# Performance work log

Hardware: AMD Instinct MI355X
Metric: run time of the kernel (lower is better)

## Reference

```python
import jax, jax.numpy as jnp
import numpy as np

B, C, T, N, KS = 32, 64, 12, 1024, 3
OUT = 64


def _gconv_layer(x, Lk, theta, b):
    # x: [B, i, T, N], Lk: [ks, N, N], theta: [i, c, ks], b: [1, c, 1, 1]
    x_c = jnp.einsum('knm,bitm->bitkn', Lk, x)        # graph diffusion
    x_gc = jnp.einsum('iok,bitkn->botn', theta, x_c) + b  # channel mix + bias
    return jax.nn.relu(x_gc + x)                      # residual + relu


def setup_inputs() -> dict:
    key = jax.random.key(0)
    ks = jax.random.split(key, 8)
    return {
        'x': jax.random.normal(ks[0], (B, C, T, N), dtype=jnp.float32),
        'Lk': jax.random.normal(ks[1], (KS, N, N), dtype=jnp.float32) * 0.05,
        'theta1': jax.random.normal(ks[2], (C, C, KS), dtype=jnp.float32) * 0.1,
        'b1': jax.random.normal(ks[3], (1, C, 1, 1), dtype=jnp.float32) * 0.1,
        'theta2': jax.random.normal(ks[4], (C, C, KS), dtype=jnp.float32) * 0.1,
        'b2': jax.random.normal(ks[5], (1, C, 1, 1), dtype=jnp.float32) * 0.1,
        'fc_w': jax.random.normal(ks[6], (OUT, C), dtype=jnp.float32) * 0.1,
        'fc_b': jax.random.normal(ks[7], (OUT,), dtype=jnp.float32) * 0.1,
    }


def reference(x, Lk, theta1, b1, theta2, b2, fc_w, fc_b):
    x1 = _gconv_layer(x, Lk, theta1, b1)
    x2 = _gconv_layer(x1, Lk, theta2, b2)
    # permute [B, c, T, N] -> [B, T, N, c], then Linear(c -> OUT)
    x2 = jnp.transpose(x2, (0, 2, 3, 1))
    return x2 @ fc_w.T + fc_b
```

## Files before the change

kernel.cpp:

```cpp
#include <hip/hip_runtime.h>

typedef unsigned short ushort_t;
typedef unsigned long long u64;
typedef short short8 __attribute__((ext_vector_type(8)));
typedef float f32x4 __attribute__((ext_vector_type(4)));

#define B_   32
#define C_   64
#define T_   12
#define N_   1024
#define KS_  3
#define KC_  3072
#define RPB  768
#define NT_  48
#define BM_  192
#define LBUF 57344
#define ABYT 24576
#define BPLN 16384

__device__ __forceinline__ float bf2f(ushort_t u) {
  union { unsigned u; float f; } v; v.u = ((unsigned)u) << 16; return v.f;
}
__device__ __forceinline__ ushort_t f2bf(float f) {
  union { float f; unsigned u; } v; v.f = f;
  unsigned r = v.u + 0x7FFFu + ((v.u >> 16) & 1u);
  return (ushort_t)(r >> 16);
}

__device__ __forceinline__ void gload16(const ushort_t* g, ushort_t* l) {
  __builtin_amdgcn_global_load_lds(
      (const __attribute__((address_space(1))) unsigned int*)g,
      (__attribute__((address_space(3))) unsigned int*)l, 16, 0, 0);
}

__global__ void prep_th(const float* __restrict__ th1, const float* __restrict__ th2,
                        ushort_t* __restrict__ out) {
  int id = blockIdx.x * 256 + threadIdx.x;
  if (id >= 24576) return;
  int l = id / 12288, rem = id % 12288;
  int k = rem / 4096;
  int o = (rem >> 6) & 63;
  int i = rem & 63;
  const float* th = l ? th2 : th1;
  out[id] = f2bf(th[(i * 64 + o) * 3 + k]);
}

__global__ void prep_bt(const float* __restrict__ Lk, ushort_t* __restrict__ Bt) {
  int id = blockIdx.x * 256 + threadIdx.x;
  int k = id >> 17, rem = id & 131071;
  int n = rem >> 7, mc = rem & 127;
  int m = mc << 3;
  const float* src = Lk + ((k * N_ + n) * N_ + m);
  float4 v0 = *(const float4*)src;
  float4 v1 = *(const float4*)(src + 4);
  short8 o8;
  o8[0] = (short)f2bf(v0.x); o8[1] = (short)f2bf(v0.y);
  o8[2] = (short)f2bf(v0.z); o8[3] = (short)f2bf(v0.w);
  o8[4] = (short)f2bf(v1.x); o8[5] = (short)f2bf(v1.y);
  o8[6] = (short)f2bf(v1.z); o8[7] = (short)f2bf(v1.w);
  *(short8*)&Bt[n * KC_ + k * N_ + m] = o8;
}

template<int IN_BF16>
__global__ __launch_bounds__(256, 2)
void mix_mfma(const void* __restrict__ in, const ushort_t* __restrict__ thA,
              ushort_t* __restrict__ Y, int b0) {
  const int bid = blockIdx.x;
  const int mq = bid & 3;
  const int bt = bid >> 2;
  const int bl = bt / 12, t = bt % 12;
  const int b = b0 + bl;
  const int tid = threadIdx.x;
  const int wv = tid >> 6, lane = tid & 63;
  const int l15 = lane & 15, l4 = lane >> 4;
  const int m0 = mq * 256 + wv * 64;

  const ushort_t* xg_b = (const ushort_t*)in;
  const float*    xg_f = (const float*)in;

  short8 bfr[4][2];
  #pragma unroll
  for (int mf = 0; mf < 4; ++mf) {
    const int m = m0 + mf * 16 + l15;
    #pragma unroll
    for (int ks = 0; ks < 2; ++ks) {
      #pragma unroll
      for (int j = 0; j < 8; ++j) {
        const int i = ks * 32 + l4 * 8 + j;
        const size_t adr = ((size_t)(b * C_ + i) * T_ + t) * N_ + m;
        ushort_t v = IN_BF16 ? xg_b[adr] : f2bf(xg_f[adr]);
        bfr[mf][ks][j] = (short)v;
      }
    }
  }

  const size_t rbase = (size_t)(bt * C_);
  #pragma unroll
  for (int k = 0; k < 3; ++k) {
    short8 afr[4][2];
    #pragma unroll
    for (int of = 0; of < 4; ++of)
      #pragma unroll
      for (int ks = 0; ks < 2; ++ks)
        afr[of][ks] = *(const short8*)&thA[(size_t)(k * 64 + of * 16 + l15) * 64 + ks * 32 + l4 * 8];

    f32x4 acc[4][4] = {};
    #pragma unroll
    for (int ks = 0; ks < 2; ++ks)
      #pragma unroll
      for (int of = 0; of < 4; ++of)
        #pragma unroll
        for (int mf = 0; mf < 4; ++mf)
          acc[of][mf] = __builtin_amdgcn_mfma_f32_16x16x32_bf16(afr[of][ks], bfr[mf][ks], acc[of][mf], 0, 0, 0);

    #pragma unroll
    for (int of = 0; of < 4; ++of)
      #pragma unroll
      for (int mf = 0; mf < 4; ++mf)
        #pragma unroll
        for (int r = 0; r < 4; ++r) {
          const int o = of * 16 + l4 * 4 + r;
          Y[(rbase + o) * KC_ + k * N_ + m0 + mf * 16 + l15] = f2bf(acc[of][mf][r]);
        }
  }
}


#define MFMA12(g)                                                                           \
  acc[3*(g)+0][0] = __builtin_amdgcn_mfma_f32_16x16x32_bf16(a0, b0, acc[3*(g)+0][0],0,0,0); \
  acc[3*(g)+0][1] = __builtin_amdgcn_mfma_f32_16x16x32_bf16(a0, b1, acc[3*(g)+0][1],0,0,0); \
  acc[3*(g)+0][2] = __builtin_amdgcn_mfma_f32_16x16x32_bf16(a0, b2, acc[3*(g)+0][2],0,0,0); \
  acc[3*(g)+0][3] = __builtin_amdgcn_mfma_f32_16x16x32_bf16(a0, b3, acc[3*(g)+0][3],0,0,0); \
  acc[3*(g)+1][0] = __builtin_amdgcn_mfma_f32_16x16x32_bf16(a1, b0, acc[3*(g)+1][0],0,0,0); \
  acc[3*(g)+1][1] = __builtin_amdgcn_mfma_f32_16x16x32_bf16(a1, b1, acc[3*(g)+1][1],0,0,0); \
  acc[3*(g)+1][2] = __builtin_amdgcn_mfma_f32_16x16x32_bf16(a1, b2, acc[3*(g)+1][2],0,0,0); \
  acc[3*(g)+1][3] = __builtin_amdgcn_mfma_f32_16x16x32_bf16(a1, b3, acc[3*(g)+1][3],0,0,0); \
  acc[3*(g)+2][0] = __builtin_amdgcn_mfma_f32_16x16x32_bf16(a2, b0, acc[3*(g)+2][0],0,0,0); \
  acc[3*(g)+2][1] = __builtin_amdgcn_mfma_f32_16x16x32_bf16(a2, b1, acc[3*(g)+2][1],0,0,0); \
  acc[3*(g)+2][2] = __builtin_amdgcn_mfma_f32_16x16x32_bf16(a2, b2, acc[3*(g)+2][2],0,0,0); \
  acc[3*(g)+2][3] = __builtin_amdgcn_mfma_f32_16x16x32_bf16(a2, b3, acc[3*(g)+2][3],0,0,0);

#define STAGE_A(kt, j) gload16(gA##j + (size_t)(kt) * 64,                                   \
    (ushort_t*)(lp + (((kt) & 1) ? LBUF : 0) + (j) * 8192 + wofs))
#define STAGE_B(kt, j) gload16(gB##j + (size_t)(kt) * 64,                                   \
    (ushort_t*)(lp + (((kt) & 1) ? LBUF : 0) + ABYT + (j) * 8192 + wofs))

#define LD8(p) (*(const short8*)(p))

template<int RES_BF16>
__global__ __launch_bounds__(512, 2)
void gemm8p(const ushort_t* __restrict__ Y, const ushort_t* __restrict__ Bt,
            const void* __restrict__ res, const float* __restrict__ bias,
            ushort_t* __restrict__ outb, int batch0) {
  const int nwg = gridDim.x;
  int orig = blockIdx.x;
  int q8 = nwg >> 3;
  int wg = (orig & 7) * q8 + (orig >> 3);
  const int mtile = wg >> 2, ntile = wg & 3;

  const int tid = threadIdx.x;
  const int wid = tid >> 6, lane = tid & 63;
  const int wm = wid >> 2, wn = wid & 3;
  const int l15 = lane & 15, l4 = lane >> 4;

  __shared__ ushort_t LDSU[LBUF];
  char* lp = (char*)LDSU;

  const int row0 = mtile * BM_;
  const int n0 = ntile * 256;
  const int wofs = wid * 1024;

  const int lam = lane >> 2, lc = lane & 3;
  const ushort_t *gA0, *gA1, *gA2, *gB0, *gB1, *gB2, *gB3;
  {
    int p, s, row, colel;
    p = 0 * 128 + wid * 16 + lam; s = p >= 192 ? 1 : 0; row = p - s * 192;
    colel = (lc * 8) ^ (((row >> 3) & 1) << 4);
    gA0 = Y + (size_t)(row0 + row) * KC_ + s * 32 + colel;
    p = 1 * 128 + wid * 16 + lam; s = p >= 192 ? 1 : 0; row = p - s * 192;
    colel = (lc * 8) ^ (((row >> 3) & 1) << 4);
    gA1 = Y + (size_t)(row0 + row) * KC_ + s * 32 + colel;
    p = 2 * 128 + wid * 16 + lam; s = p >= 192 ? 1 : 0; row = p - s * 192;
    colel = (lc * 8) ^ (((row >> 3) & 1) << 4);
    gA2 = Y + (size_t)(row0 + row) * KC_ + s * 32 + colel;
    p = 0 * 128 + wid * 16 + lam; s = p >> 8; row = p & 255;
    colel = (lc * 8) ^ (((row >> 3) & 1) << 4);
    gB0 = Bt + (size_t)(n0 + row) * KC_ + s * 32 + colel;
    p = 1 * 128 + wid * 16 + lam; s = p >> 8; row = p & 255;
    colel = (lc * 8) ^ (((row >> 3) & 1) << 4);
    gB1 = Bt + (size_t)(n0 + row) * KC_ + s * 32 + colel;
    p = 2 * 128 + wid * 16 + lam; s = p >> 8; row = p & 255;
    colel = (lc * 8) ^ (((row >> 3) & 1) << 4);
    gB2 = Bt + (size_t)(n0 + row) * KC_ + s * 32 + colel;
    p = 3 * 128 + wid * 16 + lam; s = p >> 8; row = p & 255;
    colel = (lc * 8) ^ (((row >> 3) & 1) << 4);
    gB3 = Bt + (size_t)(n0 + row) * KC_ + s * 32 + colel;
  }

  const int swz = ((l15 >> 3) & 1) << 5;
  const int a_base = (wm * 16 + l15) * 64 + ((l4 * 16) ^ swz);
  const int b_base = ABYT + (wn * 16 + l15) * 64 + ((l4 * 16) ^ swz);

  STAGE_B(0, 0); STAGE_B(0, 1); STAGE_B(0, 2); STAGE_B(0, 3);
  STAGE_A(0, 0); STAGE_A(0, 1); STAGE_A(0, 2);
  STAGE_B(1, 0); STAGE_B(1, 1); STAGE_B(1, 2); STAGE_B(1, 3);
  STAGE_A(1, 0); STAGE_A(1, 1);
  asm volatile("s_waitcnt vmcnt(6)" ::: "memory");
  __builtin_amdgcn_s_barrier();

  f32x4 acc[6][4] = {};
  short8 b0, b1, b2, b3;

  for (int u = 0; u < NT_; ++u) {
    const char* abp = lp + ((u & 1) ? LBUF : 0) + a_base;
    const char* bbp = lp + ((u & 1) ? LBUF : 0) + b_base;

    {
      short8 a0 = LD8(abp);
      short8 a1 = LD8(abp + 2048);
      short8 a2 = LD8(abp + 4096);
      b0 = LD8(bbp);  b1 = LD8(bbp + 4096);  b2 = LD8(bbp + 8192);  b3 = LD8(bbp + 12288);
      if (u + 1 < NT_) STAGE_A(u + 1, 2);
      __builtin_amdgcn_s_barrier();
      __builtin_amdgcn_s_setprio(1);
      MFMA12(0)
      __builtin_amdgcn_s_setprio(0);
      __builtin_amdgcn_s_barrier();
    }
    {
      short8 a0 = LD8(abp + 6144);
      short8 a1 = LD8(abp + 8192);
      short8 a2 = LD8(abp + 10240);
      if (u + 2 < NT_) { STAGE_B(u + 2, 0); STAGE_B(u + 2, 1); }
      __builtin_amdgcn_s_barrier();
      __builtin_amdgcn_s_setprio(1);
      MFMA12(1)
      __builtin_amdgcn_s_setprio(0);
      __builtin_amdgcn_s_barrier();
    }
    {
      short8 a0 = LD8(abp + 12288);
      short8 a1 = LD8(abp + 12288 + 2048);
      short8 a2 = LD8(abp + 12288 + 4096);
      b0 = LD8(bbp + BPLN);  b1 = LD8(bbp + BPLN + 4096);
      b2 = LD8(bbp + BPLN + 8192);  b3 = LD8(bbp + BPLN + 12288);
      __builtin_amdgcn_s_barrier();
      __builtin_amdgcn_s_setprio(1);
      MFMA12(0)
      __builtin_amdgcn_s_setprio(0);
      __builtin_amdgcn_s_barrier();
    }
    {
      short8 a0 = LD8(abp + 12288 + 6144);
      short8 a1 = LD8(abp + 12288 + 8192);
      short8 a2 = LD8(abp + 12288 + 10240);
      if (u + 2 < NT_) {
        STAGE_B(u + 2, 2); STAGE_B(u + 2, 3);
        STAGE_A(u + 2, 0); STAGE_A(u + 2, 1);
        asm volatile("s_waitcnt vmcnt(6)" ::: "memory");
      } else if (u + 2 == NT_) {
        asm volatile("s_waitcnt vmcnt(0)" ::: "memory");
      }
      __builtin_amdgcn_s_barrier();
      __builtin_amdgcn_s_setprio(1);
      MFMA12(1)
      __builtin_amdgcn_s_setprio(0);
      __builtin_amdgcn_s_barrier();
    }
  }

  const float*    resf = (const float*)res;
  const ushort_t* resb = (const ushort_t*)res;
  const int gb = batch0 + (mtile >> 2);
  const int rowb0 = (mtile & 3) * BM_;
  const int colb = n0 + wn * 16 + l15;
  #pragma unroll
  for (int mf = 0; mf < 6; ++mf) {
    #pragma unroll
    for (int r = 0; r < 4; ++r) {
      int rl = mf * 32 + wm * 16 + l4 * 4 + r;
      int rowb = rowb0 + rl;
      int t = rowb >> 6, o = rowb & 63;
      float bs = bias[o];
      size_t base = ((size_t)(gb * C_ + o) * T_ + t) * N_;
      #pragma unroll
      for (int nf = 0; nf < 4; ++nf) {
        int col = colb + nf * 64;
        float rv = RES_BF16 ? bf2f(resb[base + col]) : resf[base + col];
        float v = acc[mf][nf][r] + bs + rv;
        v = fmaxf(v, 0.0f);
        outb[base + col] = f2bf(v);
      }
    }
  }
}

__global__ __launch_bounds__(256, 2)
void fc_kernel(const ushort_t* __restrict__ x2, const float* __restrict__ fw,
               const float* __restrict__ fb, float* __restrict__ out) {
  int bid = blockIdx.x;
  int nt = bid & 15, btid = bid >> 4;
  int t = btid % 12, b = btid / 12;
  int n0 = nt << 6;
  int tid = threadIdx.x;
  __shared__ float xt[64 * 64];
  __shared__ float wl[64 * 64];
  #pragma unroll
  for (int j = 0; j < 2; ++j) {
    int c = tid + j * 256;
    int row = c >> 3, col = (c & 7) << 3;
    short8 v = *(const short8*)&x2[((b * C_ + row) * T_ + t) * N_ + n0 + col];
    #pragma unroll
    for (int q = 0; q < 8; ++q) xt[row * 64 + col + q] = bf2f((ushort_t)v[q]);
  }
  #pragma unroll
  for (int j = 0; j < 4; ++j) {
    int c = tid + j * 256;
    int o2 = c >> 4, o4 = (c & 15) << 2;
    float4 v = *(const float4*)&fw[o2 * 64 + o4];
    wl[(o4 + 0) * 64 + o2] = v.x; wl[(o4 + 1) * 64 + o2] = v.y;
    wl[(o4 + 2) * 64 + o2] = v.z; wl[(o4 + 3) * 64 + o2] = v.w;
  }
  __syncthreads();
  int p = tid & 31, ng = tid >> 5;
  float a0[8] = {}, a1[8] = {};
  for (int o = 0; o < 64; ++o) {
    float w0 = wl[o * 64 + p], w1 = wl[o * 64 + p + 32];
    float4 xa = *(const float4*)&xt[o * 64 + ng * 8];
    float4 xb = *(const float4*)&xt[o * 64 + ng * 8 + 4];
    float xv[8] = {xa.x, xa.y, xa.z, xa.w, xb.x, xb.y, xb.z, xb.w};
    #pragma unroll
    for (int j = 0; j < 8; ++j) { a0[j] = fmaf(w0, xv[j], a0[j]); a1[j] = fmaf(w1, xv[j], a1[j]); }
  }
  float fb0 = fb[p], fb1 = fb[p + 32];
  int obase = (b * T_ + t) * N_ + n0 + ng * 8;
  #pragma unroll
  for (int j = 0; j < 8; ++j) {
    out[(obase + j) * 64 + p]      = a0[j] + fb0;
    out[(obase + j) * 64 + p + 32] = a1[j] + fb1;
  }
}

extern "C" void kernel_launch(void* const* d_in, const int* in_sizes, int n_in,
                              void* d_out, int out_size, void* d_ws, size_t ws_size,
                              hipStream_t stream) {
  const float* x   = (const float*)d_in[0];
  const float* Lk  = (const float*)d_in[1];
  const float* th1 = (const float*)d_in[2];
  const float* b1  = (const float*)d_in[3];
  const float* th2 = (const float*)d_in[4];
  const float* b2  = (const float*)d_in[5];
  const float* fcw = (const float*)d_in[6];
  const float* fcb = (const float*)d_in[7];

  char* ws = (char*)d_ws;
  size_t off = 0;
  auto alloc = [&](size_t bytes) { size_t p = off; off += (bytes + 255) & ~(size_t)255; return p; };
  size_t oBt = alloc((size_t)KC_ * N_ * 2);
  size_t oTh = alloc((size_t)2 * 3 * 64 * 64 * 2);
  size_t oX2 = alloc((size_t)B_ * C_ * T_ * N_ * 2);
  size_t perB = (size_t)RPB * KC_ * 2;
  size_t avail = ws_size > off ? ws_size - off : 0;
  int NB = (int)(avail / perB);
  if (NB > B_) NB = B_;
  if (NB < 1) NB = 1;

  ushort_t* Bt = (ushort_t*)(ws + oBt);
  ushort_t* Th = (ushort_t*)(ws + oTh);
  ushort_t* X2 = (ushort_t*)(ws + oX2);
  ushort_t* Yb = (ushort_t*)(ws + off);
  ushort_t* X1 = (ushort_t*)d_out;

  prep_th<<<96, 256, 0, stream>>>(th1, th2, Th);
  prep_bt<<<1536, 256, 0, stream>>>(Lk, Bt);

  for (int b0 = 0; b0 < B_; b0 += NB) {
    int nb = (b0 + NB <= B_) ? NB : (B_ - b0);
    mix_mfma<0><<<nb * 48, 256, 0, stream>>>((const void*)x, Th, Yb, b0);
    gemm8p<0><<<dim3(16 * nb), 512, 0, stream>>>(Yb, Bt, (const void*)x, b1, X1, b0);
  }
  for (int b0 = 0; b0 < B_; b0 += NB) {
    int nb = (b0 + NB <= B_) ? NB : (B_ - b0);
    mix_mfma<1><<<nb * 48, 256, 0, stream>>>((const void*)X1, Th + 12288, Yb, b0);
    gemm8p<1><<<dim3(16 * nb), 512, 0, stream>>>(Yb, Bt, (const void*)X1, b2, X2, b0);
  }
  fc_kernel<<<32 * 12 * 16, 256, 0, stream>>>(X2, fcw, fcb, (float*)d_out);
}
```

Baseline: 503.6 us.

## Restructure GEMM main loop to load all fragments then issue MFMAs in one burst

Replaces the four-phase interleaved schedule, which had barriers between each MFMA group, with one phase per k-tile. Each tile waits on global loads, reads all A/B fragments from LDS, barriers, issues all next-tile global-to-LDS copies, then runs all 48 MFMAs. This cuts barrier count per iteration from eight to two. In exchange it holds more fragment registers at once and gives up the finer overlap of LDS reads with MFMA work.

```diff
diff --git a/kernel.cpp b/kernel.cpp
--- a/kernel.cpp
+++ b/kernel.cpp
@@ -126,20 +126,6 @@
 }
 
 
-#define MFMA12(g)                                                                           \
-  acc[3*(g)+0][0] = __builtin_amdgcn_mfma_f32_16x16x32_bf16(a0, b0, acc[3*(g)+0][0],0,0,0); \
-  acc[3*(g)+0][1] = __builtin_amdgcn_mfma_f32_16x16x32_bf16(a0, b1, acc[3*(g)+0][1],0,0,0); \
-  acc[3*(g)+0][2] = __builtin_amdgcn_mfma_f32_16x16x32_bf16(a0, b2, acc[3*(g)+0][2],0,0,0); \
-  acc[3*(g)+0][3] = __builtin_amdgcn_mfma_f32_16x16x32_bf16(a0, b3, acc[3*(g)+0][3],0,0,0); \
-  acc[3*(g)+1][0] = __builtin_amdgcn_mfma_f32_16x16x32_bf16(a1, b0, acc[3*(g)+1][0],0,0,0); \
-  acc[3*(g)+1][1] = __builtin_amdgcn_mfma_f32_16x16x32_bf16(a1, b1, acc[3*(g)+1][1],0,0,0); \
-  acc[3*(g)+1][2] = __builtin_amdgcn_mfma_f32_16x16x32_bf16(a1, b2, acc[3*(g)+1][2],0,0,0); \
-  acc[3*(g)+1][3] = __builtin_amdgcn_mfma_f32_16x16x32_bf16(a1, b3, acc[3*(g)+1][3],0,0,0); \
-  acc[3*(g)+2][0] = __builtin_amdgcn_mfma_f32_16x16x32_bf16(a2, b0, acc[3*(g)+2][0],0,0,0); \
-  acc[3*(g)+2][1] = __builtin_amdgcn_mfma_f32_16x16x32_bf16(a2, b1, acc[3*(g)+2][1],0,0,0); \
-  acc[3*(g)+2][2] = __builtin_amdgcn_mfma_f32_16x16x32_bf16(a2, b2, acc[3*(g)+2][2],0,0,0); \
-  acc[3*(g)+2][3] = __builtin_amdgcn_mfma_f32_16x16x32_bf16(a2, b3, acc[3*(g)+2][3],0,0,0);
-
 #define STAGE_A(kt, j) gload16(gA##j + (size_t)(kt) * 64,                                   \
     (ushort_t*)(lp + (((kt) & 1) ? LBUF : 0) + (j) * 8192 + wofs))
 #define STAGE_B(kt, j) gload16(gB##j + (size_t)(kt) * 64,                                   \
@@ -204,69 +190,53 @@
   STAGE_B(0, 0); STAGE_B(0, 1); STAGE_B(0, 2); STAGE_B(0, 3);
   STAGE_A(0, 0); STAGE_A(0, 1); STAGE_A(0, 2);
   STAGE_B(1, 0); STAGE_B(1, 1); STAGE_B(1, 2); STAGE_B(1, 3);
-  STAGE_A(1, 0); STAGE_A(1, 1);
-  asm volatile("s_waitcnt vmcnt(6)" ::: "memory");
-  __builtin_amdgcn_s_barrier();
+  STAGE_A(1, 0); STAGE_A(1, 1); STAGE_A(1, 2);
 
   f32x4 acc[6][4] = {};
-  short8 b0, b1, b2, b3;
 
   for (int u = 0; u < NT_; ++u) {
     const char* abp = lp + ((u & 1) ? LBUF : 0) + a_base;
     const char* bbp = lp + ((u & 1) ? LBUF : 0) + b_base;
 
-    {
-      short8 a0 = LD8(abp);
-      short8 a1 = LD8(abp + 2048);
-      short8 a2 = LD8(abp + 4096);
-      b0 = LD8(bbp);  b1 = LD8(bbp + 4096);  b2 = LD8(bbp + 8192);  b3 = LD8(bbp + 12288);
-      if (u + 1 < NT_) STAGE_A(u + 1, 2);
-      __builtin_amdgcn_s_barrier();
-      __builtin_amdgcn_s_setprio(1);
-      MFMA12(0)
-      __builtin_amdgcn_s_setprio(0);
-      __builtin_amdgcn_s_barrier();
+    if (u < NT_ - 1) {
+      asm volatile("s_waitcnt vmcnt(7)" ::: "memory");
+    } else {
+      asm volatile("s_waitcnt vmcnt(0)" ::: "memory");
     }
-    {
-      short8 a0 = LD8(abp + 6144);
-      short8 a1 = LD8(abp + 8192);
-      short8 a2 = LD8(abp + 10240);
-      if (u + 2 < NT_) { STAGE_B(u + 2, 0); STAGE_B(u + 2, 1); }
-      __builtin_amdgcn_s_barrier();
-      __builtin_amdgcn_s_setprio(1);
-      MFMA12(1)
-      __builtin_amdgcn_s_setprio(0);
-      __builtin_amdgcn_s_barrier();
+    __builtin_amdgcn_s_barrier();
+    __builtin_amdgcn_sched_barrier(0);
+
+    short8 Af[2][6], Bf[2][4];
+    #pragma unroll
+    for (int s = 0; s < 2; ++s)
+      #pragma unroll
+      for (int m = 0; m < 6; ++m)
+        Af[s][m] = LD8(abp + s * 12288 + m * 2048);
+    #pragma unroll
+    for (int s = 0; s < 2; ++s)
+      #pragma unroll
+      for (int n = 0; n < 4; ++n)
+        Bf[s][n] = LD8(bbp + s * BPLN + n * 4096);
+
+    asm volatile("s_waitcnt lgkmcnt(0)" ::: "memory");
+    __builtin_amdgcn_sched_barrier(0);
+    __builtin_amdgcn_s_barrier();
+    __builtin_amdgcn_sched_barrier(0);
+
+    if (u + 2 < NT_) {
+      STAGE_B(u + 2, 0); STAGE_B(u + 2, 1); STAGE_B(u + 2, 2); STAGE_B(u + 2, 3);
+      STAGE_A(u + 2, 0); STAGE_A(u + 2, 1); STAGE_A(u + 2, 2);
     }
-    {
-      short8 a0 = LD8(abp + 12288);
-      short8 a1 = LD8(abp + 12288 + 2048);
-      short8 a2 = LD8(abp + 12288 + 4096);
-      b0 = LD8(bbp + BPLN);  b1 = LD8(bbp + BPLN + 4096);
-      b2 = LD8(bbp + BPLN + 8192);  b3 = LD8(bbp + BPLN + 12288);
-      __builtin_amdgcn_s_barrier();
-      __builtin_amdgcn_s_setprio(1);
-      MFMA12(0)
-      __builtin_amdgcn_s_setprio(0);
-      __builtin_amdgcn_s_barrier();
-    }
-    {
-      short8 a0 = LD8(abp + 12288 + 6144);
-      short8 a1 = LD8(abp + 12288 + 8192);
-      short8 a2 = LD8(abp + 12288 + 10240);
-      if (u + 2 < NT_) {
-        STAGE_B(u + 2, 2); STAGE_B(u + 2, 3);
-        STAGE_A(u + 2, 0); STAGE_A(u + 2, 1);
-        asm volatile("s_waitcnt vmcnt(6)" ::: "memory");
-      } else if (u + 2 == NT_) {
-        asm volatile("s_waitcnt vmcnt(0)" ::: "memory");
-      }
-      __builtin_amdgcn_s_barrier();
-      __builtin_amdgcn_s_setprio(1);
-      MFMA12(1)
-      __builtin_amdgcn_s_setprio(0);
-      __builtin_amdgcn_s_barrier();
-    }
+
+    __builtin_amdgcn_s_setprio(1);
+    #pragma unroll
+    for (int s = 0; s < 2; ++s)
+      #pragma unroll
+      for (int m = 0; m < 6; ++m)
+        #pragma unroll
+        for (int n = 0; n < 4; ++n)
+          acc[m][n] = __builtin_amdgcn_mfma_f32_16x16x32_bf16(Af[s][m], Bf[s][n], acc[m][n], 0, 0, 0);
+    __builtin_amdgcn_s_setprio(0);
   }
 
   const float*    resf = (const float*)res;
```

Result: slower. 527.2 us (+4.7%).
